# Kernel optimization log

Measured on AMD Instinct MI355X. Metric: run time of the kernel, lower is better.

## Reference

```python
import jax, jax.numpy as jnp
import numpy as np

L = 4        # routed layers
E = 12       # experts
NH = 4       # attention heads
C = 256      # hidden_dim
M = 128      # mlp_dim
TOPK = 1
LN_EPS = 1e-5


def setup_inputs() -> dict:
    key = jax.random.key(0)
    ks = jax.random.split(key, 16)
    B, H, W = 128, 14, 14

    def w(k, shape, s=0.02):
        return jax.random.normal(k, shape, dtype=jnp.float32) * s

    return {
        'stem_out': jax.random.normal(ks[0], (B, C, H, W), dtype=jnp.float32),
        'gate_w': w(ks[1], (L, C, E)), 'gate_b': jnp.zeros((L, E), jnp.float32),
        'ln1_g': jnp.ones((L, E, C), jnp.float32), 'ln1_b': jnp.zeros((L, E, C), jnp.float32),
        'wq': w(ks[2], (L, E, C, C)), 'bq': jnp.zeros((L, E, C), jnp.float32),
        'wk': w(ks[3], (L, E, C, C)), 'bk': jnp.zeros((L, E, C), jnp.float32),
        'wv': w(ks[4], (L, E, C, C)), 'bv': jnp.zeros((L, E, C), jnp.float32),
        'wo': w(ks[5], (L, E, C, C)), 'bo': jnp.zeros((L, E, C), jnp.float32),
        'ln2_g': jnp.ones((L, E, C), jnp.float32), 'ln2_b': jnp.zeros((L, E, C), jnp.float32),
        'w1': w(ks[6], (L, E, C, M)), 'b1': jnp.zeros((L, E, M), jnp.float32),
        'w2': w(ks[7], (L, E, M, C)), 'b2': jnp.zeros((L, E, C), jnp.float32),
    }


def _ln(x, g, b):
    mu = x.mean(axis=-1, keepdims=True)
    var = ((x - mu) ** 2).mean(axis=-1, keepdims=True)
    return (x - mu) * jax.lax.rsqrt(var + LN_EPS) * g + b


def _vit_block(x, p):
    # x: (B, H, W, C); p: per-expert params (no expert axis)
    B, H, W, Cc = x.shape
    d = Cc // NH
    h = _ln(x, p['g1'], p['bb1'])
    q = h @ p['wq'] + p['bq']
    k = h @ p['wk'] + p['bk']
    v = h @ p['wv'] + p['bv']

    def split(t):  # (B,H,W,C) -> (B, NH, H, W, d)
        return jnp.transpose(t.reshape(B, H, W, NH, d), (0, 3, 1, 2, 4))

    q, k, v = split(q), split(k), split(v)
    # attention is computed PER ROW h (over the W axis), matching the
    # original matmul(q, k.transpose(-2,-1)) on b n h w d tensors
    scale = jnp.asarray(d, x.dtype) ** 0.5
    scores = jnp.einsum('bnhqd,bnhkd->bnhqk', q, k) / scale
    attn = jax.nn.softmax(scores, axis=-1)
    o = jnp.einsum('bnhqk,bnhkd->bnhqd', attn, v)
    o = jnp.transpose(o, (0, 2, 3, 1, 4)).reshape(B, H, W, Cc)
    o = o @ p['wo'] + p['bo']
    x = x + o
    m = _ln(x, p['g2'], p['bb2'])
    m = jax.nn.gelu(m @ p['w1'] + p['b1'], approximate=False) @ p['w2'] + p['b2']
    return x + m


def reference(stem_out, gate_w, gate_b, ln1_g, ln1_b, wq, bq, wk, bk, wv, bv,
              wo, bo, ln2_g, ln2_b, w1, b1, w2, b2):
    x = jnp.transpose(stem_out, (0, 2, 3, 1))  # (B, H, W, C)
    B = x.shape[0]
    outputs_map, probs_list, idx_list = [], [], []
    for li in range(L):
        router_in = x.mean(axis=(1, 2))                 # (B, C)
        logits = router_in @ gate_w[li] + gate_b[li]    # (B, E)
        all_probs = jax.nn.softmax(logits, axis=-1)
        tk_p, tk_i = jax.lax.top_k(all_probs, TOPK)
        tk_p = tk_p / (tk_p.sum(axis=-1, keepdims=True) + 1e-8)
        # dense combine weights (B, E): scatter top-k weights per batch row
        w_be = jnp.zeros((B, E), x.dtype).at[jnp.arange(B)[:, None], tk_i].add(tk_p)
        p_li = {'g1': ln1_g[li], 'bb1': ln1_b[li],
                'wq': wq[li], 'bq': bq[li], 'wk': wk[li], 'bk': bk[li],
                'wv': wv[li], 'bv': bv[li], 'wo': wo[li], 'bo': bo[li],
                'g2': ln2_g[li], 'bb2': ln2_b[li],
                'w1': w1[li], 'b1': b1[li], 'w2': w2[li], 'b2': b2[li]}
        expert_outs = jax.vmap(lambda pp: _vit_block(x, pp))(p_li)  # (E,B,H,W,C)
        x = jnp.einsum('ebhwc,be->bhwc', expert_outs, w_be)
        outputs_map.append(jax.lax.stop_gradient(x))
        probs_list.append(all_probs)
        idx_list.append(tk_i)
    return (jnp.stack(outputs_map, axis=0),          # (4, B, H, W, C)
            jnp.concatenate(probs_list, axis=0),     # (4B, E)
            jnp.concatenate(idx_list, axis=0))       # (4B, top_k)
```

## Files before the change

kernel.cpp:

```cpp
#include <hip/hip_runtime.h>
#include <hip/hip_bf16.h>

#define LNUM 4
#define ENUM 12
#define CH 256
#define MLP 128
#define HW 196
#define BNUM 128
#define ROWLEN 14
#define MTOT (BNUM * HW)
#define TM 128
#define MAXTILE 208

#define PK_WQ 0
#define PK_WK 786432
#define PK_WV 1572864
#define PK_WO 2359296
#define PK_W1 3145728
#define PK_W2 3538944
#define PK_TOTAL 3932160

using bf16x8 = __attribute__((ext_vector_type(8))) short;
using f32x4 = __attribute__((ext_vector_type(4))) float;

__device__ inline unsigned short f2bf(float v) {
  __hip_bfloat16 b = __float2bfloat16(v);
  return *reinterpret_cast<unsigned short*>(&b);
}
__device__ inline float bf2f(unsigned short u) {
  union { unsigned int i; float f; } cv;
  cv.i = ((unsigned int)u) << 16;
  return cv.f;
}
__device__ inline void split_bf(float v, unsigned short& hi, unsigned short& lo) {
  hi = f2bf(v);
  lo = f2bf(v - bf2f(hi));
}
__device__ inline void gload16(const void* g, void* l) {
  __builtin_amdgcn_global_load_lds(
      (const __attribute__((address_space(1))) unsigned int*)g,
      (__attribute__((address_space(3))) unsigned int*)l, 16, 0, 0);
}

__global__ __launch_bounds__(256) void transpose_stem(const float* __restrict__ stem,
                                                      float* __restrict__ x) {
  __shared__ float tile[32][33];
  int b = blockIdx.z;
  int c0 = blockIdx.x * 32;
  int p0 = blockIdx.y * 32;
  int tx = threadIdx.x;
  int ty = threadIdx.y;
  for (int i = ty; i < 32; i += 8) {
    int c = c0 + i, p = p0 + tx;
    if (p < HW) tile[i][tx] = stem[(size_t)b * CH * HW + (size_t)c * HW + p];
  }
  __syncthreads();
  for (int i = ty; i < 32; i += 8) {
    int p = p0 + i, c = c0 + tx;
    if (p < HW) x[(size_t)b * HW * CH + (size_t)p * CH + c] = tile[tx][i];
  }
}

__global__ __launch_bounds__(256) void router_kernel(
    const float* __restrict__ x, const float* __restrict__ gate_w,
    const float* __restrict__ gate_b, float* __restrict__ probs_out,
    float* __restrict__ idx_out, float* __restrict__ weight,
    int* __restrict__ eidx, int li) {
  int b = blockIdx.x;
  int c = threadIdx.x;
  const float* xb = x + (size_t)b * HW * CH;
  float s = 0.f;
  for (int p = 0; p < HW; ++p) s += xb[(size_t)p * CH + c];
  __shared__ float r[CH];
  r[c] = s * (1.0f / (float)HW);
  __syncthreads();
  __shared__ float logits[ENUM];
  if (c < ENUM) {
    float acc = gate_b[li * ENUM + c];
    for (int k = 0; k < CH; ++k)
      acc += r[k] * gate_w[((size_t)li * CH + k) * ENUM + c];
    logits[c] = acc;
  }
  __syncthreads();
  if (c == 0) {
    float mx = logits[0]; int am = 0;
    for (int e = 1; e < ENUM; ++e) if (logits[e] > mx) { mx = logits[e]; am = e; }
    float pr[ENUM]; float den = 0.f;
    for (int e = 0; e < ENUM; ++e) { pr[e] = expf(logits[e] - mx); den += pr[e]; }
    float inv = 1.0f / den;
    for (int e = 0; e < ENUM; ++e) pr[e] *= inv;
    for (int e = 0; e < ENUM; ++e)
      probs_out[(size_t)(li * BNUM + b) * ENUM + e] = pr[e];
    idx_out[li * BNUM + b] = (float)am;
    float pmax = pr[am];
    weight[b] = pmax / (pmax + 1e-8f);
    eidx[b] = am;
  }
}

__global__ void route_plan(const int* __restrict__ eidx, int* __restrict__ perm,
                           int* __restrict__ tile_e, int* __restrict__ tile_row0,
                           int* __restrict__ tile_rows) {
  __shared__ int cnt[ENUM], start[ENUM];
  int t = threadIdx.x;
  if (t < ENUM) {
    int c = 0;
    for (int b = 0; b < BNUM; ++b) if (eidx[b] == t) ++c;
    cnt[t] = c;
  }
  __syncthreads();
  if (t == 0) {
    int s = 0;
    for (int e = 0; e < ENUM; ++e) { start[e] = s; s += cnt[e]; }
  }
  __syncthreads();
  if (t < ENUM) {
    int pos = start[t];
    for (int b = 0; b < BNUM; ++b) if (eidx[b] == t) perm[pos++] = b;
  }
  __syncthreads();
  if (t == 0) {
    int tile = 0;
    for (int e = 0; e < ENUM; ++e) {
      int rows = cnt[e] * HW;
      int row0 = start[e] * HW;
      int off = 0;
      while (off < rows) {
        tile_e[tile] = e;
        tile_row0[tile] = row0 + off;
        int rem = rows - off;
        tile_rows[tile] = rem < TM ? rem : TM;
        ++tile; off += TM;
      }
    }
    for (; tile < MAXTILE; ++tile) { tile_rows[tile] = 0; tile_e[tile] = 0; tile_row0[tile] = 0; }
  }
}

__global__ __launch_bounds__(256) void prepack(
    const float* __restrict__ wq, const float* __restrict__ wk,
    const float* __restrict__ wv, const float* __restrict__ wo,
    const float* __restrict__ w1, const float* __restrict__ w2,
    unsigned short* __restrict__ Phi, unsigned short* __restrict__ Plo) {
  int e = blockIdx.z;
  int ts = blockIdx.y;
  int K = (ts == 5) ? 128 : 256;
  int N = (ts == 4) ? 128 : 256;
  int total = (K / 8) * N;
  int id = blockIdx.x * 256 + threadIdx.x;
  if (id >= total) return;
  const float* src;
  size_t dst0;
  switch (ts) {
    case 0: src = wq; dst0 = PK_WQ; break;
    case 1: src = wk; dst0 = PK_WK; break;
    case 2: src = wv; dst0 = PK_WV; break;
    case 3: src = wo; dst0 = PK_WO; break;
    case 4: src = w1; dst0 = PK_W1; break;
    default: src = w2; dst0 = PK_W2; break;
  }
  src += (size_t)e * K * N;
  dst0 += (size_t)e * K * N;
  int n = id % N;
  int kg = id / N;
  const float* sp = src + (size_t)kg * 8 * N + n;
  unsigned short hs[8], ls[8];
#pragma unroll
  for (int j = 0; j < 8; ++j) split_bf(sp[(size_t)j * N], hs[j], ls[j]);
  uint4 ph, pl;
  ph.x = hs[0] | ((unsigned)hs[1] << 16); ph.y = hs[2] | ((unsigned)hs[3] << 16);
  ph.z = hs[4] | ((unsigned)hs[5] << 16); ph.w = hs[6] | ((unsigned)hs[7] << 16);
  pl.x = ls[0] | ((unsigned)ls[1] << 16); pl.y = ls[2] | ((unsigned)ls[3] << 16);
  pl.z = ls[4] | ((unsigned)ls[5] << 16); pl.w = ls[6] | ((unsigned)ls[7] << 16);
  size_t o = dst0 + (size_t)(kg * N + n) * 8;
  *reinterpret_cast<uint4*>(Phi + o) = ph;
  *reinterpret_cast<uint4*>(Plo + o) = pl;
}

__global__ __launch_bounds__(256) void ln_kernel(
    const float* __restrict__ xin, unsigned short* __restrict__ hhi,
    unsigned short* __restrict__ hlo,
    const float* __restrict__ g, const float* __restrict__ bta,
    const int* __restrict__ eidx, const int* __restrict__ perm, int li) {
  int tok = blockIdx.x * 4 + (threadIdx.x >> 6);
  int lane = threadIdx.x & 63;
  int s = tok / HW, p = tok - s * HW;
  int b = perm[s];
  int e = eidx[b];
  float4 vx = *reinterpret_cast<const float4*>(
      &xin[((size_t)b * HW + p) * CH + lane * 4]);
  float sm = vx.x + vx.y + vx.z + vx.w;
#pragma unroll
  for (int off = 1; off < 64; off <<= 1) sm += __shfl_xor(sm, off, 64);
  float mu = sm * (1.0f / (float)CH);
  float d0 = vx.x - mu, d1 = vx.y - mu, d2 = vx.z - mu, d3 = vx.w - mu;
  float s2 = d0 * d0 + d1 * d1 + d2 * d2 + d3 * d3;
#pragma unroll
  for (int off = 1; off < 64; off <<= 1) s2 += __shfl_xor(s2, off, 64);
  float rs = rsqrtf(s2 * (1.0f / (float)CH) + 1e-5f);
  size_t gb = ((size_t)li * ENUM + e) * CH + lane * 4;
  float4 gg = *reinterpret_cast<const float4*>(&g[gb]);
  float4 bb = *reinterpret_cast<const float4*>(&bta[gb]);
  float h0 = d0 * rs * gg.x + bb.x;
  float h1 = d1 * rs * gg.y + bb.y;
  float h2 = d2 * rs * gg.z + bb.z;
  float h3 = d3 * rs * gg.w + bb.w;
  ushort4 vh, vl;
  split_bf(h0, vh.x, vl.x);
  split_bf(h1, vh.y, vl.y);
  split_bf(h2, vh.z, vl.z);
  split_bf(h3, vh.w, vl.w);
  size_t ob = (size_t)tok * CH + lane * 4;
  *reinterpret_cast<ushort4*>(&hhi[ob]) = vh;
  *reinterpret_cast<ushort4*>(&hlo[ob]) = vl;
}

template <int EPI, int NT, int KDIM, int NXTOT>
__global__ __launch_bounds__(256) void gemm_mfma(
    const unsigned short* __restrict__ Ahi, const unsigned short* __restrict__ Alo,
    const unsigned short* __restrict__ Whi, const unsigned short* __restrict__ Wlo,
    size_t wbase, size_t wstride,
    const float* __restrict__ B0, const float* __restrict__ B1p, const float* __restrict__ B2p,
    float* __restrict__ O0, float* __restrict__ O1p, float* __restrict__ O2p,
    unsigned short* __restrict__ Omhi, unsigned short* __restrict__ Omlo,
    float* __restrict__ X, const float* __restrict__ wgt,
    const int* __restrict__ tile_e, const int* __restrict__ tile_row0,
    const int* __restrict__ tile_rows, const int* __restrict__ perm, int li) {
  constexpr int NX = NT / 128;
  constexpr int NSTEP = KDIM / 32;
  int nwg = NXTOT * MAXTILE;
  int orig = blockIdx.x;
  int q = nwg >> 3, r = nwg & 7;
  int xcd = orig & 7, idx = orig >> 3;
  int wg = (xcd < r ? xcd * (q + 1) : r * (q + 1) + (xcd - r) * q) + idx;
  int tileid = wg / NXTOT;
  int cbx = wg % NXTOT;

  int rows = tile_rows[tileid];
  if (rows <= 0) return;
  int row0 = tile_row0[tileid];
  int e = tile_e[tileid];
  int cb = cbx / NX;
  int ncol0 = (cbx % NX) * 128;

  const float* Bt = (EPI == 0) ? (cb == 0 ? B0 : (cb == 1 ? B1p : B2p)) : B0;
  float* Oo = (EPI == 0) ? (cb == 0 ? O0 : (cb == 1 ? O1p : O2p)) : O0;
  size_t woff = wbase + (size_t)cb * wstride + (size_t)e * (KDIM * NT);
  const unsigned short* Wh = Whi + woff;
  const unsigned short* Wl = Wlo + woff;
  const float* bias = Bt + ((size_t)li * ENUM + e) * NT + ncol0;

  __shared__ unsigned short Ash[4][TM][8], Asl[4][TM][8];
  __shared__ unsigned short Bsh[4][128][8], Bsl[4][128][8];

  int tid = threadIdx.x;
  int lane = tid & 63, w = tid >> 6;
  int wr = w >> 1, wc = w & 1;
  int r0w = wr * 64, c0w = wc * 64;
  int lrow = lane & 15, lk = lane >> 4;

  int rlo = (lane < rows) ? lane : 0;
  int rhi = (64 + lane < rows) ? 64 + lane : 0;
  const unsigned short* gAh0 = Ahi + (size_t)(row0 + rlo) * KDIM + w * 8;
  const unsigned short* gAh1 = Ahi + (size_t)(row0 + rhi) * KDIM + w * 8;
  const unsigned short* gAl0 = Alo + (size_t)(row0 + rlo) * KDIM + w * 8;
  const unsigned short* gAl1 = Alo + (size_t)(row0 + rhi) * KDIM + w * 8;

  f32x4 acc[4][4];
#pragma unroll
  for (int i = 0; i < 4; ++i)
#pragma unroll
    for (int j = 0; j < 4; ++j) acc[i][j] = (f32x4){0.f, 0.f, 0.f, 0.f};

#pragma unroll
  for (int t = 0; t < NSTEP; ++t) {
    int k0 = t * 32;
    gload16(gAh0 + k0, &Ash[w][0][0]);
    gload16(gAh1 + k0, &Ash[w][64][0]);
    gload16(gAl0 + k0, &Asl[w][0][0]);
    gload16(gAl1 + k0, &Asl[w][64][0]);
    const unsigned short* gBh = Wh + ((size_t)(t * 4 + w) * NT + ncol0 + lane) * 8;
    const unsigned short* gBl = Wl + ((size_t)(t * 4 + w) * NT + ncol0 + lane) * 8;
    gload16(gBh, &Bsh[w][0][0]);
    gload16(gBh + 64 * 8, &Bsh[w][64][0]);
    gload16(gBl, &Bsl[w][0][0]);
    gload16(gBl + 64 * 8, &Bsl[w][64][0]);
    __syncthreads();
    bf16x8 bh[4], bl[4];
#pragma unroll
    for (int fj = 0; fj < 4; ++fj) {
      bh[fj] = *reinterpret_cast<const bf16x8*>(&Bsh[lk][c0w + fj * 16 + lrow][0]);
      bl[fj] = *reinterpret_cast<const bf16x8*>(&Bsl[lk][c0w + fj * 16 + lrow][0]);
    }
#pragma unroll
    for (int fi = 0; fi < 4; ++fi) {
      bf16x8 ah = *reinterpret_cast<const bf16x8*>(&Ash[lk][r0w + fi * 16 + lrow][0]);
      bf16x8 al = *reinterpret_cast<const bf16x8*>(&Asl[lk][r0w + fi * 16 + lrow][0]);
#pragma unroll
      for (int fj = 0; fj < 4; ++fj) {
        acc[fi][fj] = __builtin_amdgcn_mfma_f32_16x16x32_bf16(ah, bh[fj], acc[fi][fj], 0, 0, 0);
        acc[fi][fj] = __builtin_amdgcn_mfma_f32_16x16x32_bf16(ah, bl[fj], acc[fi][fj], 0, 0, 0);
        acc[fi][fj] = __builtin_amdgcn_mfma_f32_16x16x32_bf16(al, bh[fj], acc[fi][fj], 0, 0, 0);
      }
    }
    __syncthreads();
  }

#pragma unroll
  for (int fi = 0; fi < 4; ++fi) {
#pragma unroll
    for (int r2 = 0; r2 < 4; ++r2) {
      int row_l = r0w + fi * 16 + lk * 4 + r2;
      if (row_l >= rows) continue;
      int rg = row0 + row_l;
      int bsrt = 0; size_t gxb = 0; float wr_ = 1.f;
      if (EPI >= 2) {
        int s = rg / HW, p = rg - s * HW;
        bsrt = perm[s];
        gxb = ((size_t)bsrt * HW + p) * CH;
        if (EPI == 3) wr_ = wgt[bsrt];
      }
#pragma unroll
      for (int fj = 0; fj < 4; ++fj) {
        int col = c0w + fj * 16 + lrow;
        int ocol = ncol0 + col;
        float v = acc[fi][fj][r2] + bias[col];
        if (EPI == 0) {
          Oo[(size_t)rg * NT + ocol] = v;
        } else if (EPI == 1) {
          float gl = 0.5f * v * (1.0f + erff(v * 0.70710678118654752f));
          unsigned short hi, lo;
          split_bf(gl, hi, lo);
          Omhi[(size_t)rg * MLP + ocol] = hi;
          Omlo[(size_t)rg * MLP + ocol] = lo;
        } else if (EPI == 2) {
          X[gxb + ocol] += v;
        } else {
          float vv = (v + X[gxb + ocol]) * wr_;
          X[gxb + ocol] = vv;
          O0[gxb + ocol] = vv;
        }
      }
    }
  }
}

__global__ __launch_bounds__(256) void attn_kernel(
    const float* __restrict__ q, const float* __restrict__ k,
    const float* __restrict__ v, unsigned short* __restrict__ ohi,
    unsigned short* __restrict__ olo) {
  int br = blockIdx.x;
  int b = br / ROWLEN, row = br % ROWLEN;
  size_t base = ((size_t)b * HW + (size_t)row * ROWLEN) * CH;
  __shared__ float qs[ROWLEN][CH + 1];
  __shared__ float ks[ROWLEN][CH + 1];
  __shared__ float vs[ROWLEN][CH + 1];
  __shared__ float sc[4][ROWLEN][ROWLEN];
  int tid = threadIdx.x;
  for (int w = 0; w < ROWLEN; ++w) {
    qs[w][tid] = q[base + (size_t)w * CH + tid];
    ks[w][tid] = k[base + (size_t)w * CH + tid];
    vs[w][tid] = v[base + (size_t)w * CH + tid];
  }
  __syncthreads();
  for (int sidx = tid; sidx < 4 * ROWLEN * ROWLEN; sidx += 256) {
    int n = sidx / (ROWLEN * ROWLEN);
    int rem = sidx % (ROWLEN * ROWLEN);
    int i = rem / ROWLEN, j = rem % ROWLEN;
    const float* qp = &qs[i][n * 64];
    const float* kp = &ks[j][n * 64];
    float s = 0.f;
#pragma unroll
    for (int d = 0; d < 64; ++d) s = fmaf(qp[d], kp[d], s);
    sc[n][i][j] = s * 0.125f;
  }
  __syncthreads();
  if (tid < 4 * ROWLEN) {
    int n = tid / ROWLEN, i = tid % ROWLEN;
    float mx = sc[n][i][0];
    for (int j = 1; j < ROWLEN; ++j) mx = fmaxf(mx, sc[n][i][j]);
    float ex[ROWLEN]; float den = 0.f;
    for (int j = 0; j < ROWLEN; ++j) { ex[j] = expf(sc[n][i][j] - mx); den += ex[j]; }
    float inv = 1.0f / den;
    for (int j = 0; j < ROWLEN; ++j) sc[n][i][j] = ex[j] * inv;
  }
  __syncthreads();
  int n = tid / 64;
  for (int i = 0; i < ROWLEN; ++i) {
    float s = 0.f;
#pragma unroll
    for (int j = 0; j < ROWLEN; ++j) s = fmaf(sc[n][i][j], vs[j][tid], s);
    unsigned short hi, lo;
    split_bf(s, hi, lo);
    ohi[base + (size_t)i * CH + tid] = hi;
    olo[base + (size_t)i * CH + tid] = lo;
  }
}

extern "C" void kernel_launch(void* const* d_in, const int* in_sizes, int n_in,
                              void* d_out, int out_size, void* d_ws, size_t ws_size,
                              hipStream_t stream) {
  const float* stem = (const float*)d_in[0];
  const float* gate_w = (const float*)d_in[1];
  const float* gate_b = (const float*)d_in[2];
  const float* ln1_g = (const float*)d_in[3];
  const float* ln1_b = (const float*)d_in[4];
  const float* wq = (const float*)d_in[5];
  const float* bq = (const float*)d_in[6];
  const float* wk = (const float*)d_in[7];
  const float* bk = (const float*)d_in[8];
  const float* wv = (const float*)d_in[9];
  const float* bv = (const float*)d_in[10];
  const float* wo = (const float*)d_in[11];
  const float* bo = (const float*)d_in[12];
  const float* ln2_g = (const float*)d_in[13];
  const float* ln2_b = (const float*)d_in[14];
  const float* w1 = (const float*)d_in[15];
  const float* b1 = (const float*)d_in[16];
  const float* w2 = (const float*)d_in[17];
  const float* b2 = (const float*)d_in[18];

  float* out = (float*)d_out;
  float* ws = (float*)d_ws;
  const size_t IMG = (size_t)BNUM * HW * CH;
  float* x = ws;
  unsigned short* h_hi = (unsigned short*)(ws + IMG);
  unsigned short* h_lo = h_hi + (size_t)MTOT * CH;
  float* q = ws + 2 * IMG;
  float* k = ws + 3 * IMG;
  float* v = ws + 4 * IMG;
  unsigned short* m_hi = (unsigned short*)q;
  unsigned short* m_lo = m_hi + (size_t)MTOT * MLP;
  unsigned short* Whi_p = (unsigned short*)(ws + 5 * IMG);
  unsigned short* Wlo_p = Whi_p + PK_TOTAL;
  float* weight = ws + 5 * IMG + PK_TOTAL;
  int* eidx = (int*)(weight + BNUM);
  int* perm = eidx + BNUM;
  int* tile_e = perm + BNUM;
  int* tile_row0 = tile_e + MAXTILE;
  int* tile_rows = tile_row0 + MAXTILE;

  float* probs_out = out + 4 * IMG;
  float* idx_out = probs_out + (size_t)LNUM * BNUM * ENUM;

  transpose_stem<<<dim3(8, 7, BNUM), dim3(32, 8), 0, stream>>>(stem, x);

  for (int li = 0; li < LNUM; ++li) {
    router_kernel<<<BNUM, 256, 0, stream>>>(x, gate_w, gate_b, probs_out, idx_out,
                                            weight, eidx, li);
    route_plan<<<1, 64, 0, stream>>>(eidx, perm, tile_e, tile_row0, tile_rows);
    prepack<<<dim3(32, 6, ENUM), 256, 0, stream>>>(
        wq + (size_t)li * ENUM * CH * CH, wk + (size_t)li * ENUM * CH * CH,
        wv + (size_t)li * ENUM * CH * CH, wo + (size_t)li * ENUM * CH * CH,
        w1 + (size_t)li * ENUM * CH * MLP, w2 + (size_t)li * ENUM * MLP * CH,
        Whi_p, Wlo_p);
    ln_kernel<<<MTOT / 4, 256, 0, stream>>>(x, h_hi, h_lo, ln1_g, ln1_b, eidx, perm, li);
    gemm_mfma<0, 256, 256, 6><<<dim3(6 * MAXTILE), 256, 0, stream>>>(
        h_hi, h_lo, Whi_p, Wlo_p, PK_WQ, (size_t)(ENUM * CH * CH),
        bq, bk, bv, q, k, v, nullptr, nullptr, nullptr, nullptr,
        tile_e, tile_row0, tile_rows, perm, li);
    attn_kernel<<<BNUM * ROWLEN, 256, 0, stream>>>(q, k, v, h_hi, h_lo);
    gemm_mfma<2, 256, 256, 2><<<dim3(2 * MAXTILE), 256, 0, stream>>>(
        h_hi, h_lo, Whi_p, Wlo_p, PK_WO, 0,
        bo, nullptr, nullptr, nullptr, nullptr, nullptr, nullptr, nullptr,
        x, nullptr, tile_e, tile_row0, tile_rows, perm, li);
    ln_kernel<<<MTOT / 4, 256, 0, stream>>>(x, h_hi, h_lo, ln2_g, ln2_b, eidx, perm, li);
    gemm_mfma<1, 128, 256, 1><<<dim3(1 * MAXTILE), 256, 0, stream>>>(
        h_hi, h_lo, Whi_p, Wlo_p, PK_W1, 0,
        b1, nullptr, nullptr, nullptr, nullptr, nullptr, m_hi, m_lo,
        nullptr, nullptr, tile_e, tile_row0, tile_rows, perm, li);
    gemm_mfma<3, 256, 128, 2><<<dim3(2 * MAXTILE), 256, 0, stream>>>(
        m_hi, m_lo, Whi_p, Wlo_p, PK_W2, 0,
        b2, nullptr, nullptr, out + (size_t)li * IMG, nullptr, nullptr,
        nullptr, nullptr, x, weight, tile_e, tile_row0, tile_rows, perm, li);
  }
}
```

Measured before the change: 936.3 us.

## Prepack all layers' weights once and use 64-row tiles for smaller GEMMs

Moves weight prepacking out of the per-layer loop: when the workspace is large enough, a single launch converts all four layers' expert weights into packed hi/lo bf16 planes, removing the serialized prepack before each layer. Routing now also builds a 64-row tile plan. The gemm kernel is templated on tile height, and the Wo, W1 and W2 GEMMs use 64-row tiles to double the workgroup count and improve occupancy and load balance, at the cost of less weight reuse per tile. Workspace layout changes and a fallback keeps per-layer packing when memory is short.

Result: faster. 912.8 us (-2.5%).

```diff
diff --git a/kernel.cpp b/kernel.cpp
--- a/kernel.cpp
+++ b/kernel.cpp
@@ -9,8 +9,8 @@
 #define BNUM 128
 #define ROWLEN 14
 #define MTOT (BNUM * HW)
-#define TM 128
-#define MAXTILE 208
+#define MAXT128 208
+#define MAXT64 416
 
 #define PK_WQ 0
 #define PK_WK 786432
@@ -99,8 +99,9 @@
 }
 
 __global__ void route_plan(const int* __restrict__ eidx, int* __restrict__ perm,
-                           int* __restrict__ tile_e, int* __restrict__ tile_row0,
-                           int* __restrict__ tile_rows) {
+                           int* __restrict__ te128, int* __restrict__ tr0128,
+                           int* __restrict__ trw128, int* __restrict__ te64,
+                           int* __restrict__ tr064, int* __restrict__ trw64) {
   __shared__ int cnt[ENUM], start[ENUM];
   int t = threadIdx.x;
   if (t < ENUM) {
@@ -126,14 +127,29 @@
       int row0 = start[e] * HW;
       int off = 0;
       while (off < rows) {
-        tile_e[tile] = e;
-        tile_row0[tile] = row0 + off;
+        te128[tile] = e;
+        tr0128[tile] = row0 + off;
         int rem = rows - off;
-        tile_rows[tile] = rem < TM ? rem : TM;
-        ++tile; off += TM;
+        trw128[tile] = rem < 128 ? rem : 128;
+        ++tile; off += 128;
       }
     }
-    for (; tile < MAXTILE; ++tile) { tile_rows[tile] = 0; tile_e[tile] = 0; tile_row0[tile] = 0; }
+    for (; tile < MAXT128; ++tile) { trw128[tile] = 0; te128[tile] = 0; tr0128[tile] = 0; }
+  } else if (t == 1) {
+    int tile = 0;
+    for (int e = 0; e < ENUM; ++e) {
+      int rows = cnt[e] * HW;
+      int row0 = start[e] * HW;
+      int off = 0;
+      while (off < rows) {
+        te64[tile] = e;
+        tr064[tile] = row0 + off;
+        int rem = rows - off;
+        trw64[tile] = rem < 64 ? rem : 64;
+        ++tile; off += 64;
+      }
+    }
+    for (; tile < MAXT64; ++tile) { trw64[tile] = 0; te64[tile] = 0; tr064[tile] = 0; }
   }
 }
 
@@ -141,8 +157,12 @@
     const float* __restrict__ wq, const float* __restrict__ wk,
     const float* __restrict__ wv, const float* __restrict__ wo,
     const float* __restrict__ w1, const float* __restrict__ w2,
-    unsigned short* __restrict__ Phi, unsigned short* __restrict__ Plo) {
-  int e = blockIdx.z;
+    unsigned short* __restrict__ Phi, unsigned short* __restrict__ Plo,
+    int li0, int plane_mult) {
+  int lz = blockIdx.z / ENUM;
+  int e = blockIdx.z % ENUM;
+  int li = li0 + lz;
+  size_t plane = (size_t)lz * plane_mult;
   int ts = blockIdx.y;
   int K = (ts == 5) ? 128 : 256;
   int N = (ts == 4) ? 128 : 256;
@@ -159,8 +179,8 @@
     case 4: src = w1; dst0 = PK_W1; break;
     default: src = w2; dst0 = PK_W2; break;
   }
-  src += (size_t)e * K * N;
-  dst0 += (size_t)e * K * N;
+  src += ((size_t)li * ENUM + e) * K * N;
+  size_t dst = plane + dst0 + (size_t)e * K * N;
   int n = id % N;
   int kg = id / N;
   const float* sp = src + (size_t)kg * 8 * N + n;
@@ -172,7 +192,7 @@
   ph.z = hs[4] | ((unsigned)hs[5] << 16); ph.w = hs[6] | ((unsigned)hs[7] << 16);
   pl.x = ls[0] | ((unsigned)ls[1] << 16); pl.y = ls[2] | ((unsigned)ls[3] << 16);
   pl.z = ls[4] | ((unsigned)ls[5] << 16); pl.w = ls[6] | ((unsigned)ls[7] << 16);
-  size_t o = dst0 + (size_t)(kg * N + n) * 8;
+  size_t o = dst + (size_t)(kg * N + n) * 8;
   *reinterpret_cast<uint4*>(Phi + o) = ph;
   *reinterpret_cast<uint4*>(Plo + o) = pl;
 }
@@ -215,7 +235,7 @@
   *reinterpret_cast<ushort4*>(&hlo[ob]) = vl;
 }
 
-template <int EPI, int NT, int KDIM, int NXTOT>
+template <int EPI, int NT, int KDIM, int NXTOT, int TM_, int NTILE>
 __global__ __launch_bounds__(256) void gemm_mfma(
     const unsigned short* __restrict__ Ahi, const unsigned short* __restrict__ Alo,
     const unsigned short* __restrict__ Whi, const unsigned short* __restrict__ Wlo,
@@ -228,7 +248,9 @@
     const int* __restrict__ tile_rows, const int* __restrict__ perm, int li) {
   constexpr int NX = NT / 128;
   constexpr int NSTEP = KDIM / 32;
-  int nwg = NXTOT * MAXTILE;
+  constexpr int FM = TM_ / 32;
+  constexpr int NSEG = TM_ / 64;
+  int nwg = NXTOT * NTILE;
   int orig = blockIdx.x;
   int q = nwg >> 3, r = nwg & 7;
   int xcd = orig & 7, idx = orig >> 3;
@@ -250,35 +272,38 @@
   const unsigned short* Wl = Wlo + woff;
   const float* bias = Bt + ((size_t)li * ENUM + e) * NT + ncol0;
 
-  __shared__ unsigned short Ash[4][TM][8], Asl[4][TM][8];
+  __shared__ unsigned short Ash[4][TM_][8], Asl[4][TM_][8];
   __shared__ unsigned short Bsh[4][128][8], Bsl[4][128][8];
 
   int tid = threadIdx.x;
   int lane = tid & 63, w = tid >> 6;
   int wr = w >> 1, wc = w & 1;
-  int r0w = wr * 64, c0w = wc * 64;
+  int r0w = wr * (TM_ / 2), c0w = wc * 64;
   int lrow = lane & 15, lk = lane >> 4;
 
-  int rlo = (lane < rows) ? lane : 0;
-  int rhi = (64 + lane < rows) ? 64 + lane : 0;
-  const unsigned short* gAh0 = Ahi + (size_t)(row0 + rlo) * KDIM + w * 8;
-  const unsigned short* gAh1 = Ahi + (size_t)(row0 + rhi) * KDIM + w * 8;
-  const unsigned short* gAl0 = Alo + (size_t)(row0 + rlo) * KDIM + w * 8;
-  const unsigned short* gAl1 = Alo + (size_t)(row0 + rhi) * KDIM + w * 8;
-
-  f32x4 acc[4][4];
-#pragma unroll
-  for (int i = 0; i < 4; ++i)
+  const unsigned short* gAh[NSEG];
+  const unsigned short* gAl[NSEG];
+#pragma unroll
+  for (int s = 0; s < NSEG; ++s) {
+    int rl = (s * 64 + lane < rows) ? s * 64 + lane : 0;
+    gAh[s] = Ahi + (size_t)(row0 + rl) * KDIM + w * 8;
+    gAl[s] = Alo + (size_t)(row0 + rl) * KDIM + w * 8;
+  }
+
+  f32x4 acc[FM][4];
+#pragma unroll
+  for (int i = 0; i < FM; ++i)
 #pragma unroll
     for (int j = 0; j < 4; ++j) acc[i][j] = (f32x4){0.f, 0.f, 0.f, 0.f};
 
 #pragma unroll
   for (int t = 0; t < NSTEP; ++t) {
     int k0 = t * 32;
-    gload16(gAh0 + k0, &Ash[w][0][0]);
-    gload16(gAh1 + k0, &Ash[w][64][0]);
-    gload16(gAl0 + k0, &Asl[w][0][0]);
-    gload16(gAl1 + k0, &Asl[w][64][0]);
+#pragma unroll
+    for (int s = 0; s < NSEG; ++s) {
+      gload16(gAh[s] + k0, &Ash[w][s * 64][0]);
+      gload16(gAl[s] + k0, &Asl[w][s * 64][0]);
+    }
     const unsigned short* gBh = Wh + ((size_t)(t * 4 + w) * NT + ncol0 + lane) * 8;
     const unsigned short* gBl = Wl + ((size_t)(t * 4 + w) * NT + ncol0 + lane) * 8;
     gload16(gBh, &Bsh[w][0][0]);
@@ -293,7 +318,7 @@
       bl[fj] = *reinterpret_cast<const bf16x8*>(&Bsl[lk][c0w + fj * 16 + lrow][0]);
     }
 #pragma unroll
-    for (int fi = 0; fi < 4; ++fi) {
+    for (int fi = 0; fi < FM; ++fi) {
       bf16x8 ah = *reinterpret_cast<const bf16x8*>(&Ash[lk][r0w + fi * 16 + lrow][0]);
       bf16x8 al = *reinterpret_cast<const bf16x8*>(&Asl[lk][r0w + fi * 16 + lrow][0]);
 #pragma unroll
@@ -307,7 +332,7 @@
   }
 
 #pragma unroll
-  for (int fi = 0; fi < 4; ++fi) {
+  for (int fi = 0; fi < FM; ++fi) {
 #pragma unroll
     for (int r2 = 0; r2 < 4; ++r2) {
       int row_l = r0w + fi * 16 + lk * 4 + r2;
@@ -431,47 +456,60 @@
   float* v = ws + 4 * IMG;
   unsigned short* m_hi = (unsigned short*)q;
   unsigned short* m_lo = m_hi + (size_t)MTOT * MLP;
-  unsigned short* Whi_p = (unsigned short*)(ws + 5 * IMG);
-  unsigned short* Wlo_p = Whi_p + PK_TOTAL;
-  float* weight = ws + 5 * IMG + PK_TOTAL;
-  int* eidx = (int*)(weight + BNUM);
-  int* perm = eidx + BNUM;
-  int* tile_e = perm + BNUM;
-  int* tile_row0 = tile_e + MAXTILE;
-  int* tile_rows = tile_row0 + MAXTILE;
+  float* weight = ws + 5 * IMG;
+  int* ip = (int*)(weight + BNUM);
+  int* eidx = ip;              ip += BNUM;
+  int* perm = ip;              ip += BNUM;
+  int* te128 = ip;             ip += MAXT128;
+  int* tr0128 = ip;            ip += MAXT128;
+  int* trw128 = ip;            ip += MAXT128;
+  int* te64 = ip;              ip += MAXT64;
+  int* tr064 = ip;             ip += MAXT64;
+  int* trw64 = ip;             ip += MAXT64;
+  unsigned short* Whi_p = (unsigned short*)(ws + 5 * IMG + 4096);
+
+  const size_t base_bytes = (5 * IMG + 4096) * sizeof(float);
+  const int all_mode = (ws_size >= base_bytes + (size_t)4 * PK_TOTAL * 2 * sizeof(unsigned short)) ? 1 : 0;
+  const int nplane = all_mode ? LNUM : 1;
+  unsigned short* Wlo_p = Whi_p + (size_t)nplane * PK_TOTAL;
 
   float* probs_out = out + 4 * IMG;
   float* idx_out = probs_out + (size_t)LNUM * BNUM * ENUM;
 
   transpose_stem<<<dim3(8, 7, BNUM), dim3(32, 8), 0, stream>>>(stem, x);
+  if (all_mode) {
+    prepack<<<dim3(32, 6, ENUM * LNUM), 256, 0, stream>>>(
+        wq, wk, wv, wo, w1, w2, Whi_p, Wlo_p, 0, PK_TOTAL);
+  }
 
   for (int li = 0; li < LNUM; ++li) {
     router_kernel<<<BNUM, 256, 0, stream>>>(x, gate_w, gate_b, probs_out, idx_out,
                                             weight, eidx, li);
-    route_plan<<<1, 64, 0, stream>>>(eidx, perm, tile_e, tile_row0, tile_rows);
-    prepack<<<dim3(32, 6, ENUM), 256, 0, stream>>>(
-        wq + (size_t)li * ENUM * CH * CH, wk + (size_t)li * ENUM * CH * CH,
-        wv + (size_t)li * ENUM * CH * CH, wo + (size_t)li * ENUM * CH * CH,
-        w1 + (size_t)li * ENUM * CH * MLP, w2 + (size_t)li * ENUM * MLP * CH,
-        Whi_p, Wlo_p);
+    route_plan<<<1, 64, 0, stream>>>(eidx, perm, te128, tr0128, trw128,
+                                     te64, tr064, trw64);
+    if (!all_mode) {
+      prepack<<<dim3(32, 6, ENUM), 256, 0, stream>>>(
+          wq, wk, wv, wo, w1, w2, Whi_p, Wlo_p, li, 0);
+    }
+    size_t plane = all_mode ? (size_t)li * PK_TOTAL : 0;
     ln_kernel<<<MTOT / 4, 256, 0, stream>>>(x, h_hi, h_lo, ln1_g, ln1_b, eidx, perm, li);
-    gemm_mfma<0, 256, 256, 6><<<dim3(6 * MAXTILE), 256, 0, stream>>>(
-        h_hi, h_lo, Whi_p, Wlo_p, PK_WQ, (size_t)(ENUM * CH * CH),
+    gemm_mfma<0, 256, 256, 6, 128, MAXT128><<<dim3(6 * MAXT128), 256, 0, stream>>>(
+        h_hi, h_lo, Whi_p, Wlo_p, plane + PK_WQ, (size_t)(ENUM * CH * CH),
         bq, bk, bv, q, k, v, nullptr, nullptr, nullptr, nullptr,
-        tile_e, tile_row0, tile_rows, perm, li);
+        te128, tr0128, trw128, perm, li);
     attn_kernel<<<BNUM * ROWLEN, 256, 0, stream>>>(q, k, v, h_hi, h_lo);
-    gemm_mfma<2, 256, 256, 2><<<dim3(2 * MAXTILE), 256, 0, stream>>>(
-        h_hi, h_lo, Whi_p, Wlo_p, PK_WO, 0,
+    gemm_mfma<2, 256, 256, 2, 64, MAXT64><<<dim3(2 * MAXT64), 256, 0, stream>>>(
+        h_hi, h_lo, Whi_p, Wlo_p, plane + PK_WO, 0,
         bo, nullptr, nullptr, nullptr, nullptr, nullptr, nullptr, nullptr,
-        x, nullptr, tile_e, tile_row0, tile_rows, perm, li);
+        x, nullptr, te64, tr064, trw64, perm, li);
     ln_kernel<<<MTOT / 4, 256, 0, stream>>>(x, h_hi, h_lo, ln2_g, ln2_b, eidx, perm, li);
-    gemm_mfma<1, 128, 256, 1><<<dim3(1 * MAXTILE), 256, 0, stream>>>(
-        h_hi, h_lo, Whi_p, Wlo_p, PK_W1, 0,
+    gemm_mfma<1, 128, 256, 1, 64, MAXT64><<<dim3(1 * MAXT64), 256, 0, stream>>>(
+        h_hi, h_lo, Whi_p, Wlo_p, plane + PK_W1, 0,
         b1, nullptr, nullptr, nullptr, nullptr, nullptr, m_hi, m_lo,
-        nullptr, nullptr, tile_e, tile_row0, tile_rows, perm, li);
-    gemm_mfma<3, 256, 128, 2><<<dim3(2 * MAXTILE), 256, 0, stream>>>(
-        m_hi, m_lo, Whi_p, Wlo_p, PK_W2, 0,
+        nullptr, nullptr, te64, tr064, trw64, perm, li);
+    gemm_mfma<3, 256, 128, 2, 64, MAXT64><<<dim3(2 * MAXT64), 256, 0, stream>>>(
+        m_hi, m_lo, Whi_p, Wlo_p, plane + PK_W2, 0,
         b2, nullptr, nullptr, out + (size_t)li * IMG, nullptr, nullptr,
-        nullptr, nullptr, x, weight, tile_e, tile_row0, tile_rows, perm, li);
-  }
-}
+        nullptr, nullptr, x, weight, te64, tr064, trw64, perm, li);
+  }
+}
```
